# Performance work log

Measured on AMD Instinct MI355X. Metric: run time of the kernel, lower is better.

Reference implementation:

```python
import jax, jax.numpy as jnp
import numpy as np

N, L, D = 32, 4096, 768
H = 12
DH = D // H
MLP_DIM = 4 * D


def setup_inputs() -> dict:
    key = jax.random.key(0)
    ks = jax.random.split(key, 12)
    xavier = jax.nn.initializers.xavier_uniform()
    inp = {
        "x": jax.random.normal(ks[0], (N, L, D), jnp.float32),
        "probe": xavier(ks[1], (1, 1, D), jnp.float32),
        # MHA projections (flax DenseGeneral layout: (d, h, dh) / out (h, dh, d))
        "wq": xavier(ks[2], (D, H, DH), jnp.float32),
        "bq": jnp.zeros((H, DH), jnp.float32),
        "wk": xavier(ks[3], (D, H, DH), jnp.float32),
        "bk": jnp.zeros((H, DH), jnp.float32),
        "wv": xavier(ks[4], (D, H, DH), jnp.float32),
        "bv": jnp.zeros((H, DH), jnp.float32),
        "wo": xavier(ks[5], (H, DH, D), jnp.float32),
        "bo": jnp.zeros((D,), jnp.float32),
        # LayerNorm
        "ln_scale": jnp.ones((D,), jnp.float32),
        "ln_bias": jnp.zeros((D,), jnp.float32),
        # MLP block
        "w1": xavier(ks[6], (D, MLP_DIM), jnp.float32),
        "b1": jax.random.normal(ks[7], (MLP_DIM,), jnp.float32) * 1e-6,
        "w2": xavier(ks[8], (MLP_DIM, D), jnp.float32),
        "b2": jax.random.normal(ks[9], (D,), jnp.float32) * 1e-6,
    }
    return inp


def _layernorm(x, scale, bias, eps=1e-6):
    mu = jnp.mean(x, axis=-1, keepdims=True)
    var = jnp.mean(jnp.square(x - mu), axis=-1, keepdims=True)
    return (x - mu) * jax.lax.rsqrt(var + eps) * scale + bias


def reference(x, probe, wq, bq, wk, bk, wv, bv, wo, bo,
              ln_scale, ln_bias, w1, b1, w2, b2):
    n, l, d = x.shape
    q_in = jnp.broadcast_to(probe, (n, 1, d))          # tile probe over batch
    q = jnp.einsum('nqd,dhe->nqhe', q_in, wq) + bq     # [n,1,h,dh]
    k = jnp.einsum('nld,dhe->nlhe', x, wk) + bk        # [n,l,h,dh]
    v = jnp.einsum('nld,dhe->nlhe', x, wv) + bv
    q = q / jnp.sqrt(jnp.asarray(DH, q.dtype))
    logits = jnp.einsum('nqhe,nlhe->nhql', q, k)       # [n,h,1,l]
    attn = jax.nn.softmax(logits, axis=-1)
    o = jnp.einsum('nhql,nlhe->nqhe', attn, v)         # [n,1,h,dh]
    xa = jnp.einsum('nqhe,hed->nqd', o, wo) + bo       # attention output [n,1,d]
    y = _layernorm(xa, ln_scale, ln_bias)
    mlp = jnp.dot(jax.nn.gelu(jnp.dot(y, w1) + b1), w2) + b2
    out = xa + mlp
    return out[:, 0]                                   # [n,d]
```

## Files before the change

### kernel.cpp

```cpp
#include <hip/hip_runtime.h>
#include <math.h>

#define N_B 32
#define L_S 4096
#define D_M 768
#define H_N 12
#define NCH 16
#define XP  776

#define WS_QHP    0
#define WS_QK     12288
#define WS_QB     21504
#define WS_MLC    21568
#define WS_SLC    27712
#define WS_XBP    33856
#define WS_OP     4752448
#define WS_XAP    4949056
#define WS_XAS    5145664
#define WS_Y      5170240
#define WS_H1P    5194816
#define WS_MACCP  5588032

__global__ __launch_bounds__(256) void qh_kernel(
    const float* __restrict__ probe, const float* __restrict__ wq,
    const float* __restrict__ bq, float* __restrict__ qhp) {
    int i = blockIdx.x * 256 + threadIdx.x;
    int ky = blockIdx.y, d0 = ky * 48;
    float acc = 0.f;
    for (int dd = 0; dd < 48; ++dd)
        acc += probe[d0 + dd] * wq[(size_t)(d0 + dd) * 768 + i];
    acc *= 0.125f;
    if (ky == 0) acc += 0.125f * bq[i];
    qhp[ky * 768 + i] = acc;
}

__global__ __launch_bounds__(256) void qk_kernel(
    const float* __restrict__ qhp, const float* __restrict__ wk,
    const float* __restrict__ bk, float* __restrict__ qk,
    float* __restrict__ qb) {
    int h = blockIdx.x, dt = blockIdx.y, t = threadIdx.x;
    __shared__ float qh_s[64];
    if (t < 64) {
        float s = 0.f;
        #pragma unroll
        for (int k = 0; k < 16; ++k) s += qhp[k * 768 + h * 64 + t];
        qh_s[t] = s;
    }
    __syncthreads();
    int d = dt * 256 + t;
    const float4* wk4 = (const float4*)(wk + (size_t)d * 768 + h * 64);
    const float4* qh4 = (const float4*)qh_s;
    float acc = 0.f;
    #pragma unroll
    for (int e4 = 0; e4 < 16; ++e4) {
        float4 w = wk4[e4], q = qh4[e4];
        acc += w.x * q.x + w.y * q.y + w.z * q.z + w.w * q.w;
    }
    qk[h * 768 + d] = acc;
    if (dt == 0 && t < 64) {
        float v = qh_s[t] * bk[h * 64 + t];
        #pragma unroll
        for (int off = 32; off > 0; off >>= 1) v += __shfl_xor(v, off);
        if (t == 0) qb[h] = v;
    }
}

__global__ __launch_bounds__(256) void attn_fused(
    const float* __restrict__ x, const float* __restrict__ qk,
    const float* __restrict__ qb, float* __restrict__ xbp,
    float* __restrict__ mlc, float* __restrict__ slc) {
    __shared__ __align__(16) float qk_s[12 * XP];
    __shared__ __align__(16) float xs[2 * 4 * XP];
    __shared__ float lg_s[64], w_s[64], qb_s[16], ms_s[16], ss_s[16], sc_s[16];
    int lc = blockIdx.x, n = blockIdx.y, t = threadIdx.x;
    int lane = t & 63, w = t >> 6;
    size_t xbase = ((size_t)n * 4096 + lc * 256) * 768;

    for (int i = t; i < 12 * 192; i += 256) {
        int hh = i / 192, c = i % 192;
        *(float4*)&qk_s[hh * XP + c * 4] = ((const float4*)qk)[i];
    }
    if (t < 12) { qb_s[t] = qb[t]; ms_s[t] = -1e30f; ss_s[t] = 0.f; }
    {
        const float4* s0 = (const float4*)(x + xbase);
        for (int j = t; j < 768; j += 256)
            *(float4*)&xs[(j / 192) * XP + (j % 192) * 4] = s0[j];
    }
    float4 acc4[12];
    #pragma unroll
    for (int h = 0; h < 12; ++h) acc4[h] = make_float4(0.f, 0.f, 0.f, 0.f);
    int r1 = t & 3, q1 = (t >> 2) & 3, h1 = t >> 4;
    __syncthreads();

    int p = 0;
    for (int it = 0; it < 64; ++it) {
        if (w == 3 && it + 1 < 64) {
            const float4* src = (const float4*)(x + xbase + (size_t)(it + 1) * 3072);
            #pragma unroll
            for (int j = 0; j < 12; ++j) {
                int f = lane + 64 * j;
                float4 v = src[f];
                *(float4*)&xs[(p ^ 1) * 4 * XP + (f / 192) * XP + (f % 192) * 4] = v;
            }
        }
        if (t < 192) {
            const float4* xr = (const float4*)&xs[p * 4 * XP + r1 * XP];
            const float4* kr = (const float4*)&qk_s[h1 * XP];
            float a = 0.f;
            #pragma unroll 8
            for (int s = 0; s < 48; ++s) {
                int idx = s * 4 + q1;
                float4 xv = xr[idx], kv = kr[idx];
                a += xv.x * kv.x + xv.y * kv.y + xv.z * kv.z + xv.w * kv.w;
            }
            a += __shfl_xor(a, 4);
            a += __shfl_xor(a, 8);
            if (q1 == 0) lg_s[r1 * 16 + h1] = a + qb_s[h1];
        }
        __syncthreads();
        if (t < 12) {
            float l0 = lg_s[0 * 16 + t], l1 = lg_s[1 * 16 + t];
            float l2 = lg_s[2 * 16 + t], l3 = lg_s[3 * 16 + t];
            float mt = fmaxf(fmaxf(l0, l1), fmaxf(l2, l3));
            float mo = ms_s[t];
            float mn = fmaxf(mo, mt);
            float sc = __expf(mo - mn);
            float e0 = __expf(l0 - mn), e1 = __expf(l1 - mn);
            float e2 = __expf(l2 - mn), e3 = __expf(l3 - mn);
            w_s[0 * 16 + t] = e0; w_s[1 * 16 + t] = e1;
            w_s[2 * 16 + t] = e2; w_s[3 * 16 + t] = e3;
            ms_s[t] = mn;
            ss_s[t] = ss_s[t] * sc + (e0 + e1 + e2 + e3);
            sc_s[t] = sc;
        }
        __syncthreads();
        if (t < 192) {
            const float* xb = &xs[p * 4 * XP];
            const float4* w4 = (const float4*)w_s;
            const float4* sc4 = (const float4*)sc_s;
            float4 sa = sc4[0], sb = sc4[1], sc = sc4[2];
            acc4[0].x *= sa.x; acc4[0].y *= sa.x; acc4[0].z *= sa.x; acc4[0].w *= sa.x;
            acc4[1].x *= sa.y; acc4[1].y *= sa.y; acc4[1].z *= sa.y; acc4[1].w *= sa.y;
            acc4[2].x *= sa.z; acc4[2].y *= sa.z; acc4[2].z *= sa.z; acc4[2].w *= sa.z;
            acc4[3].x *= sa.w; acc4[3].y *= sa.w; acc4[3].z *= sa.w; acc4[3].w *= sa.w;
            acc4[4].x *= sb.x; acc4[4].y *= sb.x; acc4[4].z *= sb.x; acc4[4].w *= sb.x;
            acc4[5].x *= sb.y; acc4[5].y *= sb.y; acc4[5].z *= sb.y; acc4[5].w *= sb.y;
            acc4[6].x *= sb.z; acc4[6].y *= sb.z; acc4[6].z *= sb.z; acc4[6].w *= sb.z;
            acc4[7].x *= sb.w; acc4[7].y *= sb.w; acc4[7].z *= sb.w; acc4[7].w *= sb.w;
            acc4[8].x *= sc.x; acc4[8].y *= sc.x; acc4[8].z *= sc.x; acc4[8].w *= sc.x;
            acc4[9].x *= sc.y; acc4[9].y *= sc.y; acc4[9].z *= sc.y; acc4[9].w *= sc.y;
            acc4[10].x *= sc.z; acc4[10].y *= sc.z; acc4[10].z *= sc.z; acc4[10].w *= sc.z;
            acc4[11].x *= sc.w; acc4[11].y *= sc.w; acc4[11].z *= sc.w; acc4[11].w *= sc.w;
            #pragma unroll
            for (int l = 0; l < 4; ++l) {
                float4 xv = *(const float4*)&xb[l * XP + 4 * t];
                float4 wa = w4[l * 4], wb = w4[l * 4 + 1], wc = w4[l * 4 + 2];
                acc4[0].x += wa.x * xv.x; acc4[0].y += wa.x * xv.y; acc4[0].z += wa.x * xv.z; acc4[0].w += wa.x * xv.w;
                acc4[1].x += wa.y * xv.x; acc4[1].y += wa.y * xv.y; acc4[1].z += wa.y * xv.z; acc4[1].w += wa.y * xv.w;
                acc4[2].x += wa.z * xv.x; acc4[2].y += wa.z * xv.y; acc4[2].z += wa.z * xv.z; acc4[2].w += wa.z * xv.w;
                acc4[3].x += wa.w * xv.x; acc4[3].y += wa.w * xv.y; acc4[3].z += wa.w * xv.z; acc4[3].w += wa.w * xv.w;
                acc4[4].x += wb.x * xv.x; acc4[4].y += wb.x * xv.y; acc4[4].z += wb.x * xv.z; acc4[4].w += wb.x * xv.w;
                acc4[5].x += wb.y * xv.x; acc4[5].y += wb.y * xv.y; acc4[5].z += wb.y * xv.z; acc4[5].w += wb.y * xv.w;
                acc4[6].x += wb.z * xv.x; acc4[6].y += wb.z * xv.y; acc4[6].z += wb.z * xv.z; acc4[6].w += wb.z * xv.w;
                acc4[7].x += wb.w * xv.x; acc4[7].y += wb.w * xv.y; acc4[7].z += wb.w * xv.z; acc4[7].w += wb.w * xv.w;
                acc4[8].x += wc.x * xv.x; acc4[8].y += wc.x * xv.y; acc4[8].z += wc.x * xv.z; acc4[8].w += wc.x * xv.w;
                acc4[9].x += wc.y * xv.x; acc4[9].y += wc.y * xv.y; acc4[9].z += wc.y * xv.z; acc4[9].w += wc.y * xv.w;
                acc4[10].x += wc.z * xv.x; acc4[10].y += wc.z * xv.y; acc4[10].z += wc.z * xv.z; acc4[10].w += wc.z * xv.w;
                acc4[11].x += wc.w * xv.x; acc4[11].y += wc.w * xv.y; acc4[11].z += wc.w * xv.z; acc4[11].w += wc.w * xv.w;
            }
        }
        __syncthreads();
        p ^= 1;
    }
    size_t ob = ((size_t)(lc * 32 + n)) * 12 * 768;
    if (t < 192) {
        #pragma unroll
        for (int h = 0; h < 12; ++h)
            *(float4*)&xbp[ob + h * 768 + 4 * t] = acc4[h];
    }
    if (t < 12) {
        mlc[(n * 12 + t) * 16 + lc] = ms_s[t];
        slc[(n * 12 + t) * 16 + lc] = ss_s[t];
    }
}

__global__ __launch_bounds__(256) void oproj_kernel(
    const float* __restrict__ xbp, const float* __restrict__ mlc,
    const float* __restrict__ slc, const float* __restrict__ wv,
    const float* __restrict__ bv, float* __restrict__ op) {
    int h = blockIdx.x, kk = blockIdx.y, t = threadIdx.x;
    int d0 = kk * 96;
    __shared__ __align__(16) float wv_s[96 * 64];
    __shared__ __align__(16) float xb_s[96 * 32];
    __shared__ float scl_s[16 * 32];
    if (t < 32) {
        float M = -1e30f;
        #pragma unroll
        for (int c = 0; c < 16; ++c) M = fmaxf(M, mlc[(t * 12 + h) * 16 + c]);
        float e[16], T = 0.f;
        #pragma unroll
        for (int c = 0; c < 16; ++c) {
            e[c] = __expf(mlc[(t * 12 + h) * 16 + c] - M);
            T += slc[(t * 12 + h) * 16 + c] * e[c];
        }
        float inv = 1.f / T;
        #pragma unroll
        for (int c = 0; c < 16; ++c) scl_s[c * 32 + t] = e[c] * inv;
    }
    for (int i = t; i < 96 * 64; i += 256) {
        int d = i >> 6, e = i & 63;
        wv_s[i] = wv[(size_t)(d0 + d) * 768 + h * 64 + e];
    }
    __syncthreads();
    for (int i = t; i < 96 * 32; i += 256) {
        int d = i >> 5, nn = i & 31;
        float s = 0.f;
        #pragma unroll
        for (int lcc = 0; lcc < 16; ++lcc)
            s += xbp[(((size_t)lcc * 32 + nn) * 12 + h) * 768 + d0 + d]
               * scl_s[lcc * 32 + nn];
        xb_s[i] = s;
    }
    __syncthreads();
    int e = t & 63, ng = t >> 6;
    float acc[8] = {0, 0, 0, 0, 0, 0, 0, 0};
    for (int d = 0; d < 96; ++d) {
        float wvv = wv_s[d * 64 + e];
        const float4* xb4 = (const float4*)&xb_s[d * 32 + ng * 8];
        float4 p0 = xb4[0], p1 = xb4[1];
        acc[0] += p0.x * wvv; acc[1] += p0.y * wvv; acc[2] += p0.z * wvv; acc[3] += p0.w * wvv;
        acc[4] += p1.x * wvv; acc[5] += p1.y * wvv; acc[6] += p1.z * wvv; acc[7] += p1.w * wvv;
    }
    float bvv = (kk == 0) ? bv[h * 64 + e] : 0.f;
    #pragma unroll
    for (int k = 0; k < 8; ++k)
        op[(size_t)kk * 24576 + (size_t)(ng * 8 + k) * 768 + h * 64 + e] = acc[k] + bvv;
}

__global__ __launch_bounds__(256) void xaproj_kernel(
    const float* __restrict__ op, const float* __restrict__ wo,
    const float* __restrict__ bo, float* __restrict__ xap) {
    int dt = blockIdx.x, kk = blockIdx.y, t = threadIdx.x;
    int i0 = kk * 96;
    __shared__ __align__(16) float o_s[96 * 32];
    for (int idx = t; idx < 96 * 32; idx += 256) {
        int i = idx >> 5, nn = idx & 31;
        float s = 0.f;
        #pragma unroll
        for (int pp = 0; pp < 8; ++pp)
            s += op[(size_t)pp * 24576 + (size_t)nn * 768 + i0 + i];
        o_s[idx] = s;
    }
    __syncthreads();
    int d = dt * 256 + t;
    float acc[32];
    #pragma unroll
    for (int nn = 0; nn < 32; ++nn) acc[nn] = 0.f;
    for (int i = 0; i < 96; ++i) {
        float w = wo[(size_t)(i0 + i) * 768 + d];
        const float4* o4 = (const float4*)&o_s[i * 32];
        #pragma unroll
        for (int qq = 0; qq < 8; ++qq) {
            float4 f = o4[qq];
            acc[qq * 4 + 0] += f.x * w; acc[qq * 4 + 1] += f.y * w;
            acc[qq * 4 + 2] += f.z * w; acc[qq * 4 + 3] += f.w * w;
        }
    }
    float bov = (kk == 0) ? bo[d] : 0.f;
    #pragma unroll
    for (int nn = 0; nn < 32; ++nn)
        xap[(size_t)kk * 24576 + (size_t)nn * 768 + d] = acc[nn] + bov;
}

__global__ __launch_bounds__(256) void ln_kernel(
    const float* __restrict__ xap, const float* __restrict__ ln_scale,
    const float* __restrict__ ln_bias, float* __restrict__ xas,
    float* __restrict__ y) {
    int n = blockIdx.x, tid = threadIdx.x;
    __shared__ float xs[768];
    __shared__ float red[4];
    for (int i = tid; i < 768; i += 256) {
        float s = 0.f;
        #pragma unroll
        for (int pp = 0; pp < 8; ++pp)
            s += xap[(size_t)pp * 24576 + (size_t)n * 768 + i];
        xs[i] = s;
        xas[(size_t)n * 768 + i] = s;
    }
    __syncthreads();
    float lsum = 0.f;
    for (int i = tid; i < 768; i += 256) lsum += xs[i];
    #pragma unroll
    for (int off = 32; off > 0; off >>= 1) lsum += __shfl_xor(lsum, off);
    int wave = tid >> 6;
    if ((tid & 63) == 0) red[wave] = lsum;
    __syncthreads();
    float mu = (red[0] + red[1] + red[2] + red[3]) * (1.f / 768.f);
    __syncthreads();
    float lsq = 0.f;
    for (int i = tid; i < 768; i += 256) { float c = xs[i] - mu; lsq += c * c; }
    #pragma unroll
    for (int off = 32; off > 0; off >>= 1) lsq += __shfl_xor(lsq, off);
    if ((tid & 63) == 0) red[wave] = lsq;
    __syncthreads();
    float var = (red[0] + red[1] + red[2] + red[3]) * (1.f / 768.f);
    float rs = rsqrtf(var + 1e-6f);
    for (int i = tid; i < 768; i += 256)
        y[(size_t)n * 768 + i] = (xs[i] - mu) * rs * ln_scale[i] + ln_bias[i];
}

__global__ __launch_bounds__(256) void mlp1_kernel(
    const float* __restrict__ y, const float* __restrict__ w1,
    float* __restrict__ h1p) {
    int jt = blockIdx.x, kk = blockIdx.y, t = threadIdx.x;
    int d0 = kk * 192;
    __shared__ __align__(16) float y_s[192 * 32];
    for (int idx = t; idx < 192 * 32; idx += 256) {
        int d = idx >> 5, nn = idx & 31;
        y_s[idx] = y[(size_t)nn * 768 + d0 + d];
    }
    __syncthreads();
    int j = jt * 256 + t;
    float acc[32];
    #pragma unroll
    for (int nn = 0; nn < 32; ++nn) acc[nn] = 0.f;
    for (int d = 0; d < 192; ++d) {
        float w = w1[(size_t)(d0 + d) * 3072 + j];
        const float4* y4 = (const float4*)&y_s[d * 32];
        #pragma unroll
        for (int qq = 0; qq < 8; ++qq) {
            float4 f = y4[qq];
            acc[qq * 4 + 0] += f.x * w; acc[qq * 4 + 1] += f.y * w;
            acc[qq * 4 + 2] += f.z * w; acc[qq * 4 + 3] += f.w * w;
        }
    }
    #pragma unroll
    for (int nn = 0; nn < 32; ++nn)
        h1p[(size_t)kk * 98304 + (size_t)nn * 3072 + j] = acc[nn];
}

__global__ __launch_bounds__(256) void mlp2_kernel(
    const float* __restrict__ h1p, const float* __restrict__ b1,
    const float* __restrict__ w2, float* __restrict__ maccp) {
    int dt = blockIdx.x, kk = blockIdx.y, t = threadIdx.x;
    int j0 = kk * 192;
    __shared__ __align__(16) float h_s[192 * 32];
    for (int idx = t; idx < 192 * 32; idx += 256) {
        int j = idx >> 5, nn = idx & 31;
        float tv = b1[j0 + j];
        #pragma unroll
        for (int pp = 0; pp < 4; ++pp)
            tv += h1p[(size_t)pp * 98304 + (size_t)nn * 3072 + j0 + j];
        float u = 0.7978845608028654f * (tv + 0.044715f * tv * tv * tv);
        h_s[idx] = 0.5f * tv * (1.f + tanhf(u));
    }
    __syncthreads();
    int d = dt * 256 + t;
    float acc[32];
    #pragma unroll
    for (int nn = 0; nn < 32; ++nn) acc[nn] = 0.f;
    for (int j = 0; j < 192; ++j) {
        float w = w2[(size_t)(j0 + j) * 768 + d];
        const float4* h4 = (const float4*)&h_s[j * 32];
        #pragma unroll
        for (int qq = 0; qq < 8; ++qq) {
            float4 f = h4[qq];
            acc[qq * 4 + 0] += f.x * w; acc[qq * 4 + 1] += f.y * w;
            acc[qq * 4 + 2] += f.z * w; acc[qq * 4 + 3] += f.w * w;
        }
    }
    #pragma unroll
    for (int nn = 0; nn < 32; ++nn)
        maccp[(size_t)kk * 24576 + (size_t)nn * 768 + d] = acc[nn];
}

__global__ __launch_bounds__(256) void final_kernel(
    const float* __restrict__ xas, const float* __restrict__ b2,
    const float* __restrict__ maccp, float* __restrict__ out) {
    int n = blockIdx.x, t = threadIdx.x;
    for (int i = t; i < 768; i += 256) {
        float s = xas[(size_t)n * 768 + i] + b2[i];
        #pragma unroll
        for (int k = 0; k < 16; ++k)
            s += maccp[(size_t)k * 24576 + (size_t)n * 768 + i];
        out[(size_t)n * 768 + i] = s;
    }
}

extern "C" void kernel_launch(void* const* d_in, const int* in_sizes, int n_in,
                              void* d_out, int out_size, void* d_ws, size_t ws_size,
                              hipStream_t stream) {
    const float* x        = (const float*)d_in[0];
    const float* probe    = (const float*)d_in[1];
    const float* wq       = (const float*)d_in[2];
    const float* bq       = (const float*)d_in[3];
    const float* wk       = (const float*)d_in[4];
    const float* bk       = (const float*)d_in[5];
    const float* wv       = (const float*)d_in[6];
    const float* bv       = (const float*)d_in[7];
    const float* wo       = (const float*)d_in[8];
    const float* bo       = (const float*)d_in[9];
    const float* ln_scale = (const float*)d_in[10];
    const float* ln_bias  = (const float*)d_in[11];
    const float* w1       = (const float*)d_in[12];
    const float* b1       = (const float*)d_in[13];
    const float* w2       = (const float*)d_in[14];
    const float* b2       = (const float*)d_in[15];
    float* out = (float*)d_out;
    float* ws  = (float*)d_ws;

    float* qhp   = ws + WS_QHP;
    float* qk    = ws + WS_QK;
    float* qb    = ws + WS_QB;
    float* mlc   = ws + WS_MLC;
    float* slc   = ws + WS_SLC;
    float* xbp   = ws + WS_XBP;
    float* op    = ws + WS_OP;
    float* xap   = ws + WS_XAP;
    float* xas   = ws + WS_XAS;
    float* y     = ws + WS_Y;
    float* h1p   = ws + WS_H1P;
    float* maccp = ws + WS_MACCP;

    qh_kernel<<<dim3(3, 16), 256, 0, stream>>>(probe, wq, bq, qhp);
    qk_kernel<<<dim3(12, 3), 256, 0, stream>>>(qhp, wk, bk, qk, qb);
    attn_fused<<<dim3(NCH, 32), 256, 0, stream>>>(x, qk, qb, xbp, mlc, slc);
    oproj_kernel<<<dim3(12, 8), 256, 0, stream>>>(xbp, mlc, slc, wv, bv, op);
    xaproj_kernel<<<dim3(3, 8), 256, 0, stream>>>(op, wo, bo, xap);
    ln_kernel<<<N_B, 256, 0, stream>>>(xap, ln_scale, ln_bias, xas, y);
    mlp1_kernel<<<dim3(12, 4), 256, 0, stream>>>(y, w1, h1p);
    mlp2_kernel<<<dim3(3, 16), 256, 0, stream>>>(h1p, b1, w2, maccp);
    final_kernel<<<N_B, 256, 0, stream>>>(xas, b2, maccp, out);
}
```

Measured before the change: 845.9 us.

## Hold qk in registers in attention logits and split MLP K-dim finer

The attention kernel now keeps each thread's slice of the query-key projection in registers rather than in a 12-row shared-memory array. Each thread computes four row partial dot products, which are reduced with a four-step shuffle, and launch bounds request two blocks per CU. Separately, both MLP GEMV kernels split the reduction dimension into 16 and 64 chunks instead of 4 and 16, quadrupling their grids. This raises parallelism on the many CUs but adds more partial-sum traffic, and the workspace offset is shifted to fit the larger partials buffer.

```diff
diff --git a/kernel.cpp b/kernel.cpp
--- a/kernel.cpp
+++ b/kernel.cpp
@@ -19,7 +19,7 @@
 #define WS_XAS    5145664
 #define WS_Y      5170240
 #define WS_H1P    5194816
-#define WS_MACCP  5588032
+#define WS_MACCP  6767680
 
 __global__ __launch_bounds__(256) void qh_kernel(
     const float* __restrict__ probe, const float* __restrict__ wq,
@@ -65,20 +65,24 @@
     }
 }
 
-__global__ __launch_bounds__(256) void attn_fused(
+__global__ __launch_bounds__(256, 2) void attn_fused(
     const float* __restrict__ x, const float* __restrict__ qk,
     const float* __restrict__ qb, float* __restrict__ xbp,
     float* __restrict__ mlc, float* __restrict__ slc) {
-    __shared__ __align__(16) float qk_s[12 * XP];
     __shared__ __align__(16) float xs[2 * 4 * XP];
-    __shared__ float lg_s[64], w_s[64], qb_s[16], ms_s[16], ss_s[16], sc_s[16];
+    __shared__ __align__(16) float lg_s[64], w_s[64];
+    __shared__ __align__(16) float qb_s[16], ms_s[16], ss_s[16], sc_s[16];
     int lc = blockIdx.x, n = blockIdx.y, t = threadIdx.x;
     int lane = t & 63, w = t >> 6;
     size_t xbase = ((size_t)n * 4096 + lc * 256) * 768;
 
-    for (int i = t; i < 12 * 192; i += 256) {
-        int hh = i / 192, c = i % 192;
-        *(float4*)&qk_s[hh * XP + c * 4] = ((const float4*)qk)[i];
+    int h1 = t >> 4, q1 = t & 15;
+    float4 qk_r[12];
+    if (t < 192) {
+        const float4* qk4 = (const float4*)qk;
+        #pragma unroll
+        for (int k = 0; k < 12; ++k)
+            qk_r[k] = qk4[h1 * 192 + k * 16 + q1];
     }
     if (t < 12) { qb_s[t] = qb[t]; ms_s[t] = -1e30f; ss_s[t] = 0.f; }
     {
@@ -89,7 +93,6 @@
     float4 acc4[12];
     #pragma unroll
     for (int h = 0; h < 12; ++h) acc4[h] = make_float4(0.f, 0.f, 0.f, 0.f);
-    int r1 = t & 3, q1 = (t >> 2) & 3, h1 = t >> 4;
     __syncthreads();
 
     int p = 0;
@@ -104,18 +107,31 @@
             }
         }
         if (t < 192) {
-            const float4* xr = (const float4*)&xs[p * 4 * XP + r1 * XP];
-            const float4* kr = (const float4*)&qk_s[h1 * XP];
-            float a = 0.f;
-            #pragma unroll 8
-            for (int s = 0; s < 48; ++s) {
-                int idx = s * 4 + q1;
-                float4 xv = xr[idx], kv = kr[idx];
-                a += xv.x * kv.x + xv.y * kv.y + xv.z * kv.z + xv.w * kv.w;
+            const float* xbb = &xs[p * 4 * XP];
+            float a[4];
+            #pragma unroll
+            for (int r = 0; r < 4; ++r) {
+                const float4* xr = (const float4*)&xbb[r * XP + q1 * 4];
+                float s = 0.f;
+                #pragma unroll
+                for (int k = 0; k < 12; ++k) {
+                    float4 xv = xr[k * 16];
+                    float4 kv = qk_r[k];
+                    s += xv.x * kv.x + xv.y * kv.y + xv.z * kv.z + xv.w * kv.w;
+                }
+                a[r] = s;
             }
-            a += __shfl_xor(a, 4);
-            a += __shfl_xor(a, 8);
-            if (q1 == 0) lg_s[r1 * 16 + h1] = a + qb_s[h1];
+            #pragma unroll
+            for (int r = 0; r < 4; ++r) {
+                a[r] += __shfl_xor(a[r], 1);
+                a[r] += __shfl_xor(a[r], 2);
+                a[r] += __shfl_xor(a[r], 4);
+                a[r] += __shfl_xor(a[r], 8);
+            }
+            if (q1 == 0) {
+                #pragma unroll
+                for (int r = 0; r < 4; ++r) lg_s[r * 16 + h1] = a[r] + qb_s[h1];
+            }
         }
         __syncthreads();
         if (t < 12) {
@@ -313,9 +329,9 @@
     const float* __restrict__ y, const float* __restrict__ w1,
     float* __restrict__ h1p) {
     int jt = blockIdx.x, kk = blockIdx.y, t = threadIdx.x;
-    int d0 = kk * 192;
-    __shared__ __align__(16) float y_s[192 * 32];
-    for (int idx = t; idx < 192 * 32; idx += 256) {
+    int d0 = kk * 48;
+    __shared__ __align__(16) float y_s[48 * 32];
+    for (int idx = t; idx < 48 * 32; idx += 256) {
         int d = idx >> 5, nn = idx & 31;
         y_s[idx] = y[(size_t)nn * 768 + d0 + d];
     }
@@ -324,7 +340,7 @@
     float acc[32];
     #pragma unroll
     for (int nn = 0; nn < 32; ++nn) acc[nn] = 0.f;
-    for (int d = 0; d < 192; ++d) {
+    for (int d = 0; d < 48; ++d) {
         float w = w1[(size_t)(d0 + d) * 3072 + j];
         const float4* y4 = (const float4*)&y_s[d * 32];
         #pragma unroll
@@ -343,13 +359,13 @@
     const float* __restrict__ h1p, const float* __restrict__ b1,
     const float* __restrict__ w2, float* __restrict__ maccp) {
     int dt = blockIdx.x, kk = blockIdx.y, t = threadIdx.x;
-    int j0 = kk * 192;
-    __shared__ __align__(16) float h_s[192 * 32];
-    for (int idx = t; idx < 192 * 32; idx += 256) {
+    int j0 = kk * 48;
+    __shared__ __align__(16) float h_s[48 * 32];
+    for (int idx = t; idx < 48 * 32; idx += 256) {
         int j = idx >> 5, nn = idx & 31;
         float tv = b1[j0 + j];
         #pragma unroll
-        for (int pp = 0; pp < 4; ++pp)
+        for (int pp = 0; pp < 16; ++pp)
             tv += h1p[(size_t)pp * 98304 + (size_t)nn * 3072 + j0 + j];
         float u = 0.7978845608028654f * (tv + 0.044715f * tv * tv * tv);
         h_s[idx] = 0.5f * tv * (1.f + tanhf(u));
@@ -359,7 +375,7 @@
     float acc[32];
     #pragma unroll
     for (int nn = 0; nn < 32; ++nn) acc[nn] = 0.f;
-    for (int j = 0; j < 192; ++j) {
+    for (int j = 0; j < 48; ++j) {
         float w = w2[(size_t)(j0 + j) * 768 + d];
         const float4* h4 = (const float4*)&h_s[j * 32];
         #pragma unroll
@@ -381,7 +397,7 @@
     for (int i = t; i < 768; i += 256) {
         float s = xas[(size_t)n * 768 + i] + b2[i];
         #pragma unroll
-        for (int k = 0; k < 16; ++k)
+        for (int k = 0; k < 64; ++k)
             s += maccp[(size_t)k * 24576 + (size_t)n * 768 + i];
         out[(size_t)n * 768 + i] = s;
     }
@@ -428,7 +444,7 @@
     oproj_kernel<<<dim3(12, 8), 256, 0, stream>>>(xbp, mlc, slc, wv, bv, op);
     xaproj_kernel<<<dim3(3, 8), 256, 0, stream>>>(op, wo, bo, xap);
     ln_kernel<<<N_B, 256, 0, stream>>>(xap, ln_scale, ln_bias, xas, y);
-    mlp1_kernel<<<dim3(12, 4), 256, 0, stream>>>(y, w1, h1p);
-    mlp2_kernel<<<dim3(3, 16), 256, 0, stream>>>(h1p, b1, w2, maccp);
+    mlp1_kernel<<<dim3(12, 16), 256, 0, stream>>>(y, w1, h1p);
+    mlp2_kernel<<<dim3(3, 64), 256, 0, stream>>>(h1p, b1, w2, maccp);
     final_kernel<<<N_B, 256, 0, stream>>>(xas, b2, maccp, out);
 }
```

After: 1.030 ms. 21.7% more time.
